# Kernel tuning notes

Hardware: AMD Instinct MI355X
Metric: run time of the kernel (lower is better)

The kernel has to match this reference:

```python
import jax, jax.numpy as jnp
import numpy as np

B, N, H, T = 4096, 512, 1024, 10  # batch, input_size, hidden_size, num_iterations
NUM_OPS = 20


def setup_inputs() -> dict:
    key = jax.random.key(0)
    k1, k2, k3, k4 = jax.random.split(key, 4)
    return {
        "x": jax.random.normal(k1, (B, N, 1), jnp.float32),
        "frozen_weight": jax.random.normal(k2, (1, N, H), jnp.float32) / np.sqrt(H),
        "alpha": jax.random.normal(k3, (T, NUM_OPS), jnp.float32),
        "layer_beta": jax.random.normal(k4, (T, 2), jnp.float32),
    }


def _softshrink(x, lam):
    return jnp.where(x > lam, x - lam, jnp.where(x < -lam, x + lam, jnp.zeros_like(x)))


def _hardshrink(x, lam):
    return jnp.where(jnp.abs(x) > lam, x, jnp.zeros_like(x))


def _make_ops(lam):
    # Same 20 ops, same order as the torch ModuleList.
    return [
        lambda x: _softshrink(x, lam),                 # Softshrink(0.001/L)
        jax.nn.relu,                                   # ReLU
        lambda x: x,                                   # Identity
        lambda x: jax.nn.gelu(x, approximate=False),   # GELU (exact erf, torch default)
        jax.nn.elu,                                    # ELU
        lambda x: _hardshrink(x, lam),                 # Hardshrink(0.001/L)
        lambda x: jnp.clip(x, -1.0, 1.0),              # Hardtanh
        jax.nn.hard_swish,                             # Hardswish
        jax.nn.selu,                                   # SELU
        jax.nn.celu,                                   # CELU
        jax.nn.leaky_relu,                             # LeakyReLU (slope 0.01)
        jax.nn.log_sigmoid,                            # LogSigmoid
        lambda x: x - jnp.tanh(x),                     # Tanhshrink
        jax.nn.soft_sign,                              # Softsign
        jax.nn.softplus,                               # Softplus
        jnp.tanh,                                      # Tanh
        jax.nn.sigmoid,                                # Sigmoid
        jax.nn.hard_sigmoid,                           # Hardsigmoid
        jax.nn.silu,                                   # SiLU
        lambda x: x * jnp.tanh(jax.nn.softplus(x)),    # Mish
    ]


def _forward(x, frozen_weight, alpha, layer_beta):
    W = frozen_weight[0]                       # [N, H]
    L = jnp.linalg.norm(W, ord=2) ** 2         # spectral norm squared (Lipschitz)
    lam = 0.001 / L
    ops = _make_ops(lam)

    b = x.shape[0]
    hidden = W.shape[1]
    z = jnp.zeros((b, hidden, 1), dtype=x.dtype)
    z_prev = z
    num_iters = alpha.shape[0]
    for i in range(num_iters):
        aw = jax.nn.softmax(alpha[i])          # [20] (training path, eval_flag=False)
        bw = jax.nn.softmax(layer_beta[i])     # [2]
        # FISTA-style momentum + frozen-weight gradient step
        z_aux = z + (i / (i + 3)) * (z - z_prev)      # [B,H,1]
        Wz = jnp.einsum('nh,bho->bno', W, z_aux)      # [B,N,1]
        grad = jnp.einsum('nh,bno->bho', W, Wz - x)   # [B,H,1]
        z_g = z_aux - grad / L
        # 20-way weighted activation mixture
        z_op = aw[0] * ops[0](z_g)
        for w, op in zip(aw[1:], ops[1:]):
            z_op = z_op + w * op(z_g)
        # beta-weighted residual mix becomes z_prev; z_op becomes current_z
        z_prev = z * bw[0] + z_op * bw[1]
        z = z_op
    return z


def reference(x, frozen_weight, alpha, layer_beta):
    return _forward(x, frozen_weight, alpha, layer_beta)
```

## Files before the change

kernel.cpp:

```cpp
#include <hip/hip_runtime.h>
#include <hip/hip_bf16.h>

#define DI __device__ __forceinline__

typedef float f32x4 __attribute__((ext_vector_type(4)));
typedef __bf16 bf16x8 __attribute__((ext_vector_type(8)));
using bf16_t = __hip_bfloat16;
using ushort_t = unsigned short;

DI void gload_lds16(const void* g, void* l) {
  __builtin_amdgcn_global_load_lds(
      (const __attribute__((address_space(1))) void*)g,
      (__attribute__((address_space(3))) void*)l, 16, 0, 0);
}

DI float rcpf(float x) { return __builtin_amdgcn_rcpf(x); }

DI float act_mix(float x, const float* aw, float lam) {
  const float ax  = fabsf(x);
  const float en  = __expf(-ax);
  const float en2 = en * en;
  const float i1  = rcpf(1.0f + en);
  const float sig = (x >= 0.0f) ? i1 : en * i1;
  const float th  = copysignf((1.0f - en2) * rcpf(1.0f + en2), x);
  const float l1p = __logf(1.0f + en);
  const float sp  = fmaxf(x, 0.0f) + l1p;
  const float lsg = fminf(x, 0.0f) - l1p;
  const float q   = ((x >= 0.0f) ? en2 : 1.0f) * (i1 * i1);
  const float mish = x * (1.0f - q) * rcpf(1.0f + q);
  const float u  = 0.7071067811865476f * x;
  const float au = fabsf(u);
  const float t  = rcpf(1.0f + 0.3275911f * au);
  float poly = fmaf(t, 1.061405429f, -1.453152027f);
  poly = fmaf(t, poly, 1.421413741f);
  poly = fmaf(t, poly, -0.284496736f);
  poly = fmaf(t, poly, 0.254829592f);
  poly *= t;
  const float erfa = 1.0f - poly * __expf(-u * u);
  const float gelu = 0.5f * x * (1.0f + copysignf(erfa, x));
  const float em1  = en - 1.0f;
  const float elu  = (x > 0.0f) ? x : em1;
  const float selu = (x > 0.0f) ? 1.0507009873554805f * x : 1.7580993408473766f * em1;
  const float relu = fmaxf(x, 0.0f);
  const float t6   = fminf(fmaxf(x + 3.0f, 0.0f), 6.0f) * 0.16666666666666666f;
  const float ssh  = (x > lam) ? (x - lam) : ((x < -lam) ? (x + lam) : 0.0f);
  const float hsh  = (ax > lam) ? x : 0.0f;
  const float htan = fminf(fmaxf(x, -1.0f), 1.0f);
  const float lky  = (x >= 0.0f) ? x : 0.01f * x;
  const float ssn  = x * rcpf(1.0f + ax);
  float r = aw[0] * ssh;
  r = fmaf(aw[1],  relu,   r);
  r = fmaf(aw[2],  x,      r);
  r = fmaf(aw[3],  gelu,   r);
  r = fmaf(aw[4],  elu,    r);
  r = fmaf(aw[5],  hsh,    r);
  r = fmaf(aw[6],  htan,   r);
  r = fmaf(aw[7],  x * t6, r);
  r = fmaf(aw[8],  selu,   r);
  r = fmaf(aw[9],  elu,    r);
  r = fmaf(aw[10], lky,    r);
  r = fmaf(aw[11], lsg,    r);
  r = fmaf(aw[12], x - th, r);
  r = fmaf(aw[13], ssn,    r);
  r = fmaf(aw[14], sp,     r);
  r = fmaf(aw[15], th,     r);
  r = fmaf(aw[16], sig,    r);
  r = fmaf(aw[17], t6,     r);
  r = fmaf(aw[18], x * sig, r);
  r = fmaf(aw[19], mish,   r);
  return r;
}

__global__ void k_prep(const float* __restrict__ W, const float* __restrict__ x,
                       bf16_t* __restrict__ Whi, bf16_t* __restrict__ Wlo,
                       bf16_t* __restrict__ Wth, bf16_t* __restrict__ Wtl,
                       bf16_t* __restrict__ xh, bf16_t* __restrict__ xl) {
  int i = blockIdx.x * 256 + threadIdx.x;
  if (i < 512 * 1024) {
    float w = W[i];
    bf16_t h = __float2bfloat16(w);
    bf16_t l = __float2bfloat16(w - __bfloat162float(h));
    Whi[i] = h; Wlo[i] = l;
    int n = i >> 10, hc = i & 1023;
    Wth[hc * 512 + n] = h; Wtl[hc * 512 + n] = l;
  }
  int j = i - 512 * 1024;
  if (j >= 0 && j < 4096 * 512) {
    float v = x[j];
    bf16_t h = __float2bfloat16(v);
    xh[j] = h;
    xl[j] = __float2bfloat16(v - __bfloat162float(h));
  }
}

template <int KDIM, bool FIRST, bool WF32>
__global__ __launch_bounds__(256) void k_sqm(
    const bf16_t* __restrict__ Xhi, const bf16_t* __restrict__ Xlo,
    bf16_t* __restrict__ Chi, bf16_t* __restrict__ Clo,
    float* __restrict__ Cf,
    const float* __restrict__ pin, float* __restrict__ pout) {
  __shared__ __align__(16) ushort_t Ah[2][32 * 64], Al[2][32 * 64],
                                    Bh[2][32 * 64], Bl[2][32 * 64];
  __shared__ float red[4];
  const int tid = threadIdx.x, lane = tid & 63, wave = tid >> 6;
  const int wm = wave >> 1, wn = wave & 1;
  const int i0 = blockIdx.x * 32, j0 = blockIdx.y * 32;
  const int bid = blockIdx.y * gridDim.x + blockIdx.x;
  const int r16 = lane & 15, kg = lane >> 4;

  float s = 1.0f;
  if constexpr (!FIRST) {
    float v = pin[tid];
    for (int off = 32; off; off >>= 1) v += __shfl_down(v, off, 64);
    if ((tid & 63) == 0) red[tid >> 6] = v;
    __syncthreads();
    s = 1.0f / (red[0] + red[1] + red[2] + red[3]);
    __syncthreads();
  }

  const int row = tid >> 3;
  const int srcc = (((tid & 7) ^ (row & 7)) << 3);
  const long abase = (long)(i0 + row) * KDIM + srcc;
  const long bbase = (long)(j0 + row) * KDIM + srcc;
  const int ldst = tid * 8;

  auto stage = [&](int buf, int kt) {
    gload_lds16(Xhi + abase + kt, &Ah[buf][ldst]);
    gload_lds16(Xlo + abase + kt, &Al[buf][ldst]);
    gload_lds16(Xhi + bbase + kt, &Bh[buf][ldst]);
    gload_lds16(Xlo + bbase + kt, &Bl[buf][ldst]);
  };

  f32x4 acc = {};
  constexpr int NT = KDIM / 64;
  stage(0, 0);
  __syncthreads();
  for (int t = 0; t < NT; ++t) {
    if (t + 1 < NT) stage((t + 1) & 1, (t + 1) * 64);
    const int b = t & 1;
    const int ra = wm * 16 + r16, rb = wn * 16 + r16;
#pragma unroll
    for (int kk = 0; kk < 64; kk += 32) {
      int oa = ra * 64 + ((kk + kg * 8) ^ ((ra & 7) * 8));
      int ob = rb * 64 + ((kk + kg * 8) ^ ((rb & 7) * 8));
      bf16x8 ah = *(const bf16x8*)&Ah[b][oa];
      bf16x8 al = *(const bf16x8*)&Al[b][oa];
      bf16x8 bh = *(const bf16x8*)&Bh[b][ob];
      bf16x8 bl = *(const bf16x8*)&Bl[b][ob];
      acc = __builtin_amdgcn_mfma_f32_16x16x32_bf16(ah, bh, acc, 0, 0, 0);
      acc = __builtin_amdgcn_mfma_f32_16x16x32_bf16(ah, bl, acc, 0, 0, 0);
      acc = __builtin_amdgcn_mfma_f32_16x16x32_bf16(al, bh, acc, 0, 0, 0);
    }
    __syncthreads();
  }

  float fro = 0.0f;
#pragma unroll
  for (int r = 0; r < 4; ++r) {
    float c = acc[r] * s;
    int orow = i0 + wm * 16 + (lane >> 4) * 4 + r;
    int ocol = j0 + wn * 16 + r16;
    int idx = orow * 512 + ocol;
    bf16_t h = __float2bfloat16(c);
    Chi[idx] = h;
    Clo[idx] = __float2bfloat16(c - __bfloat162float(h));
    if constexpr (WF32) Cf[idx] = c;
    fro = fmaf(c, c, fro);
  }
  for (int off = 32; off; off >>= 1) fro += __shfl_down(fro, off, 64);
  if ((tid & 63) == 0) red[tid >> 6] = fro;
  __syncthreads();
  if (tid == 0) pout[bid] = red[0] + red[1] + red[2] + red[3];
}

__global__ __launch_bounds__(256) void k_G(const bf16_t* __restrict__ Xhi,
                                           const bf16_t* __restrict__ Xlo,
                                           bf16_t* __restrict__ G) {
  __shared__ __align__(16) ushort_t Ah[2][32 * 64], Al[2][32 * 64],
                                    Bh[2][32 * 64], Bl[2][32 * 64];
  const int tid = threadIdx.x, lane = tid & 63, wave = tid >> 6;
  const int wm = wave >> 1, wn = wave & 1;
  const int i0 = blockIdx.x * 32, j0 = blockIdx.y * 32;
  const int r16 = lane & 15, kg = lane >> 4;
  const int row = tid >> 3;
  const int srcc = (((tid & 7) ^ (row & 7)) << 3);
  const long abase = (long)(i0 + row) * 512 + srcc;
  const long bbase = (long)(j0 + row) * 512 + srcc;
  const int ldst = tid * 8;

  auto stage = [&](int buf, int kt) {
    gload_lds16(Xhi + abase + kt, &Ah[buf][ldst]);
    gload_lds16(Xlo + abase + kt, &Al[buf][ldst]);
    gload_lds16(Xhi + bbase + kt, &Bh[buf][ldst]);
    gload_lds16(Xlo + bbase + kt, &Bl[buf][ldst]);
  };

  f32x4 acc = {};
  stage(0, 0);
  __syncthreads();
  for (int t = 0; t < 8; ++t) {
    if (t + 1 < 8) stage((t + 1) & 1, (t + 1) * 64);
    const int b = t & 1;
    const int ra = wm * 16 + r16, rb = wn * 16 + r16;
#pragma unroll
    for (int kk = 0; kk < 64; kk += 32) {
      int oa = ra * 64 + ((kk + kg * 8) ^ ((ra & 7) * 8));
      int ob = rb * 64 + ((kk + kg * 8) ^ ((rb & 7) * 8));
      bf16x8 ah = *(const bf16x8*)&Ah[b][oa];
      bf16x8 al = *(const bf16x8*)&Al[b][oa];
      bf16x8 bh = *(const bf16x8*)&Bh[b][ob];
      bf16x8 bl = *(const bf16x8*)&Bl[b][ob];
      acc = __builtin_amdgcn_mfma_f32_16x16x32_bf16(ah, bh, acc, 0, 0, 0);
      acc = __builtin_amdgcn_mfma_f32_16x16x32_bf16(ah, bl, acc, 0, 0, 0);
      acc = __builtin_amdgcn_mfma_f32_16x16x32_bf16(al, bh, acc, 0, 0, 0);
    }
    __syncthreads();
  }
#pragma unroll
  for (int r = 0; r < 4; ++r) {
    int orow = i0 + wm * 16 + (lane >> 4) * 4 + r;
    int ocol = j0 + wn * 16 + r16;
    G[orow * 1024 + ocol] = __float2bfloat16(acc[r]);
  }
}

__global__ __launch_bounds__(256) void k_xw(const bf16_t* __restrict__ xh_,
                                            const bf16_t* __restrict__ xl_,
                                            const bf16_t* __restrict__ Bh_,
                                            const bf16_t* __restrict__ Bl_,
                                            const float* __restrict__ prm,
                                            bf16_t* __restrict__ out,
                                            bf16_t* __restrict__ zB,
                                            bf16_t* __restrict__ zaux1) {
  __shared__ __align__(16) ushort_t Axh[2][64 * 64], Axl[2][64 * 64],
                                    Bwh[2][64 * 64], Bwl[2][64 * 64];
  const int tid = threadIdx.x, lane = tid & 63, wave = tid >> 6;
  const int wm = wave >> 1, wn = wave & 1;
  const int m0 = blockIdx.x * 64, n0 = blockIdx.y * 64;
  const int r16 = lane & 15, kg = lane >> 4;

  auto stage = [&](int buf, int kt) {
#pragma unroll
    for (int q = 0; q < 2; ++q) {
      int lin = (tid + q * 256) * 8;
      int row = lin >> 6;
      int col = ((((lin >> 3) & 7) ^ (row & 7)) << 3);
      gload_lds16(xh_ + (long)(m0 + row) * 512 + kt + col, &Axh[buf][lin]);
      gload_lds16(xl_ + (long)(m0 + row) * 512 + kt + col, &Axl[buf][lin]);
      gload_lds16(Bh_ + (long)(n0 + row) * 512 + kt + col, &Bwh[buf][lin]);
      gload_lds16(Bl_ + (long)(n0 + row) * 512 + kt + col, &Bwl[buf][lin]);
    }
  };

  f32x4 acc[2][2] = {};
  stage(0, 0);
  __syncthreads();
  for (int t = 0; t < 8; ++t) {
    if (t + 1 < 8) stage((t + 1) & 1, (t + 1) * 64);
    const int b = t & 1;
#pragma unroll
    for (int kk = 0; kk < 64; kk += 32) {
      bf16x8 ah[2], al[2], bh[2], bl[2];
#pragma unroll
      for (int f = 0; f < 2; ++f) {
        int ra = wm * 32 + f * 16 + r16;
        int rb = wn * 32 + f * 16 + r16;
        int oa = ra * 64 + ((kk + kg * 8) ^ ((ra & 7) * 8));
        int ob = rb * 64 + ((kk + kg * 8) ^ ((rb & 7) * 8));
        ah[f] = *(const bf16x8*)&Axh[b][oa];
        al[f] = *(const bf16x8*)&Axl[b][oa];
        bh[f] = *(const bf16x8*)&Bwh[b][ob];
        bl[f] = *(const bf16x8*)&Bwl[b][ob];
      }
#pragma unroll
      for (int i = 0; i < 2; ++i)
#pragma unroll
        for (int j = 0; j < 2; ++j) {
          acc[i][j] = __builtin_amdgcn_mfma_f32_16x16x32_bf16(ah[i], bh[j], acc[i][j], 0, 0, 0);
          acc[i][j] = __builtin_amdgcn_mfma_f32_16x16x32_bf16(ah[i], bl[j], acc[i][j], 0, 0, 0);
          acc[i][j] = __builtin_amdgcn_mfma_f32_16x16x32_bf16(al[i], bh[j], acc[i][j], 0, 0, 0);
        }
    }
    __syncthreads();
  }
  const float invL = prm[21];
  const float d0 = prm[20];
  const float lam = prm[22];
  float aw[20];
#pragma unroll
  for (int k = 0; k < 20; ++k) aw[k] = prm[k];
#pragma unroll
  for (int i = 0; i < 2; ++i)
#pragma unroll
    for (int j = 0; j < 2; ++j)
#pragma unroll
      for (int r = 0; r < 4; ++r) {
        int row = m0 + wm * 32 + i * 16 + (lane >> 4) * 4 + r;
        int col = n0 + wn * 32 + j * 16 + r16;
        long idx = (long)row * 1024 + col;
        bf16_t xb = __float2bfloat16(acc[i][j][r] * invL);
        out[idx] = xb;
        float zop = act_mix(__bfloat162float(xb), aw, lam);
        zB[idx] = __float2bfloat16(zop);
        zaux1[idx] = __float2bfloat16(zop * (1.0f + d0));
      }
}

__global__ __launch_bounds__(256) void k_dot(const float* __restrict__ A0,
                                             const float* __restrict__ B,
                                             float* __restrict__ numP,
                                             float* __restrict__ denP) {
  __shared__ float redn[4], redd[4];
  const int tid = threadIdx.x;
  const int idx4 = blockIdx.x * 256 + tid;
  const f32x4 a = ((const f32x4*)A0)[idx4];
  const f32x4 b = ((const f32x4*)B)[idx4];
  float nv = a[0]*b[0] + a[1]*b[1] + a[2]*b[2] + a[3]*b[3];
  float dv = 0.0f;
#pragma unroll
  for (int q = 0; q < 4; ++q) {
    int i = idx4 * 4 + q;
    if ((i >> 9) == (i & 511)) dv += b[q];
  }
  for (int off = 32; off; off >>= 1) {
    nv += __shfl_down(nv, off, 64);
    dv += __shfl_down(dv, off, 64);
  }
  if ((tid & 63) == 0) { redn[tid >> 6] = nv; redd[tid >> 6] = dv; }
  __syncthreads();
  if (tid == 0) {
    numP[blockIdx.x] = redn[0] + redn[1] + redn[2] + redn[3];
    denP[blockIdx.x] = redd[0] + redd[1] + redd[2] + redd[3];
  }
}

__global__ __launch_bounds__(256) void k_setup(const float* __restrict__ alpha,
                                               const float* __restrict__ beta,
                                               const float* __restrict__ numP,
                                               const float* __restrict__ denP,
                                               float* __restrict__ params) {
  __shared__ float redn[4], redd[4];
  __shared__ float Lsh;
  const int tid = threadIdx.x;
  float nv = numP[tid], dv = denP[tid];
  for (int off = 32; off; off >>= 1) {
    nv += __shfl_down(nv, off, 64);
    dv += __shfl_down(dv, off, 64);
  }
  if ((tid & 63) == 0) { redn[tid >> 6] = nv; redd[tid >> 6] = dv; }
  __syncthreads();
  if (tid == 0)
    Lsh = (redn[0] + redn[1] + redn[2] + redn[3]) /
          (redd[0] + redd[1] + redd[2] + redd[3]);
  __syncthreads();
  const int t = tid;
  if (t >= 10) return;
  float L = Lsh;
  float invL = 1.0f / L;
  float lam = 0.001f * invL;
  const float* a = alpha + t * 20;
  float mx = a[0];
  for (int k = 1; k < 20; ++k) mx = fmaxf(mx, a[k]);
  float e[20], ssum = 0.0f;
  for (int k = 0; k < 20; ++k) { e[k] = expf(a[k] - mx); ssum += e[k]; }
  float inv = 1.0f / ssum;
  float* P = params + t * 32;
  for (int k = 0; k < 20; ++k) P[k] = e[k] * inv;
  float b0 = beta[t * 2], b1 = beta[t * 2 + 1];
  float bm = fmaxf(b0, b1);
  float eb0 = expf(b0 - bm), eb1 = expf(b1 - bm);
  float bw0 = eb0 / (eb0 + eb1);
  P[20] = ((float)(t + 1) / (float)(t + 4)) * bw0;
  P[21] = invL;
  P[22] = lam;
  P[23] = L;
}

template <bool LAST>
__global__ __launch_bounds__(256, 3) void k_iter(const bf16_t* __restrict__ A,
                                                 const bf16_t* __restrict__ G,
                                                 const bf16_t* __restrict__ xWs,
                                                 bf16_t* __restrict__ zauxN,
                                                 bf16_t* zB, float* zio,
                                                 const float* __restrict__ prm) {
  __shared__ __align__(16) ushort_t As[3][64 * 64], Bs[3][64 * 64];
  const int tid = threadIdx.x, lane = tid & 63, wave = tid >> 6;
  const int wm = wave >> 1, wn = wave & 1;
  const int bid = blockIdx.x;
  const int swz = (bid & 7) * 128 + (bid >> 3);
  const int m0 = (swz >> 4) * 64, n0 = (swz & 15) * 64;
  const int r16 = lane & 15, kg = lane >> 4;

  auto stage = [&](int buf, int kt) {
#pragma unroll
    for (int q = 0; q < 2; ++q) {
      int lin = (tid + q * 256) * 8;
      int row = lin >> 6;
      int col = ((((lin >> 3) & 7) ^ (row & 7)) << 3);
      gload_lds16(A + (long)(m0 + row) * 1024 + kt + col, &As[buf][lin]);
      gload_lds16(G + (long)(n0 + row) * 1024 + kt + col, &Bs[buf][lin]);
    }
  };

  f32x4 acc[2][2] = {};
  auto compute = [&](int b) {
#pragma unroll
    for (int kk = 0; kk < 64; kk += 32) {
      bf16x8 a[2], bb[2];
#pragma unroll
      for (int f = 0; f < 2; ++f) {
        int ra = wm * 32 + f * 16 + r16;
        int rb = wn * 32 + f * 16 + r16;
        a[f]  = *(const bf16x8*)&As[b][ra * 64 + ((kk + kg * 8) ^ ((ra & 7) * 8))];
        bb[f] = *(const bf16x8*)&Bs[b][rb * 64 + ((kk + kg * 8) ^ ((rb & 7) * 8))];
      }
#pragma unroll
      for (int i = 0; i < 2; ++i)
#pragma unroll
        for (int j = 0; j < 2; ++j)
          acc[i][j] = __builtin_amdgcn_mfma_f32_16x16x32_bf16(a[i], bb[j], acc[i][j], 0, 0, 0);
    }
  };

  stage(0, 0);
  stage(1, 64);
  stage(2, 128);
  asm volatile("s_waitcnt vmcnt(8)" ::: "memory");
  __builtin_amdgcn_s_barrier();
  __builtin_amdgcn_sched_barrier(0);

  for (int t = 0; t < 16; ++t) {
    compute(t % 3);
    if (t == 15) break;
    asm volatile("s_waitcnt lgkmcnt(0)" ::: "memory");
    __builtin_amdgcn_sched_barrier(0);
    __builtin_amdgcn_s_barrier();
    if (t + 3 < 16) {
      stage(t % 3, (t + 3) * 64);
      asm volatile("s_waitcnt vmcnt(8)" ::: "memory");
    } else if (t == 13) {
      asm volatile("s_waitcnt vmcnt(4)" ::: "memory");
    } else {
      asm volatile("s_waitcnt vmcnt(0)" ::: "memory");
    }
    __builtin_amdgcn_s_barrier();
    __builtin_amdgcn_sched_barrier(0);
  }
  __builtin_amdgcn_sched_barrier(0);

  const float d_i = prm[20];
  const float invL = prm[21];
  const float lam = prm[22];
  float aw[20];
#pragma unroll
  for (int k = 0; k < 20; ++k) aw[k] = prm[k];

  float xv[2][2][4], av[2][2][4], zv[2][2][4];
#pragma unroll
  for (int i = 0; i < 2; ++i)
#pragma unroll
    for (int j = 0; j < 2; ++j)
#pragma unroll
      for (int r = 0; r < 4; ++r) {
        int row = m0 + wm * 32 + i * 16 + (lane >> 4) * 4 + r;
        int col = n0 + wn * 32 + j * 16 + r16;
        long idx = (long)row * 1024 + col;
        xv[i][j][r] = __bfloat162float(xWs[idx]);
        av[i][j][r] = __bfloat162float(A[idx]);
        if (!LAST) zv[i][j][r] = __bfloat162float(zB[idx]);
      }
#pragma unroll
  for (int i = 0; i < 2; ++i)
#pragma unroll
    for (int j = 0; j < 2; ++j)
#pragma unroll
      for (int r = 0; r < 4; ++r) {
        int row = m0 + wm * 32 + i * 16 + (lane >> 4) * 4 + r;
        int col = n0 + wn * 32 + j * 16 + r16;
        long idx = (long)row * 1024 + col;
        float zg = fmaf(-acc[i][j][r], invL, av[i][j][r] + xv[i][j][r]);
        float zop = act_mix(zg, aw, lam);
        if (LAST) {
          zio[idx] = zop;
        } else {
          zB[idx] = __float2bfloat16(zop);
          zauxN[idx] = __float2bfloat16(fmaf(d_i, zop - zv[i][j][r], zop));
        }
      }
}

extern "C" void kernel_launch(void* const* d_in, const int* in_sizes, int n_in,
                              void* d_out, int out_size, void* d_ws, size_t ws_size,
                              hipStream_t stream) {
  const float* x     = (const float*)d_in[0];
  const float* W     = (const float*)d_in[1];
  const float* alpha = (const float*)d_in[2];
  const float* beta  = (const float*)d_in[3];
  float* zout = (float*)d_out;

  char* ws = (char*)d_ws;
  const size_t MB = 1u << 20;
  float* pb[11];
  for (int k = 0; k < 11; ++k) pb[k] = (float*)(ws + (size_t)k * 1024);
  float* numP   = (float*)(ws + 12 * 1024);
  float* denP   = (float*)(ws + 13 * 1024);
  float* params = (float*)(ws + 14 * 1024);
  const size_t HDR = 32768;
  float*  A0f  = (float*)(ws + HDR);
  float*  Bf   = (float*)(ws + HDR + 1 * MB);
  bf16_t* H0   = (bf16_t*)(ws + HDR + 2 * MB);
  bf16_t* L0   = (bf16_t*)(ws + HDR + 2 * MB + 512 * 1024);
  bf16_t* H1   = (bf16_t*)(ws + HDR + 3 * MB);
  bf16_t* L1   = (bf16_t*)(ws + HDR + 3 * MB + 512 * 1024);
  bf16_t* Whi  = (bf16_t*)(ws + HDR + 4 * MB);
  bf16_t* Wlo  = (bf16_t*)(ws + HDR + 5 * MB);
  bf16_t* Wth  = (bf16_t*)(ws + HDR + 6 * MB);
  bf16_t* Wtl  = (bf16_t*)(ws + HDR + 7 * MB);
  bf16_t* Gm   = (bf16_t*)(ws + HDR + 8 * MB);
  bf16_t* xh   = (bf16_t*)(ws + HDR + 10 * MB);
  bf16_t* xl   = (bf16_t*)(ws + HDR + 14 * MB);
  bf16_t* xWs  = (bf16_t*)(ws + HDR + 18 * MB);
  bf16_t* zx0  = (bf16_t*)(ws + HDR + 26 * MB);
  bf16_t* zx1  = (bf16_t*)(ws + HDR + 34 * MB);
  bf16_t* zB   = (bf16_t*)(ws + HDR + 42 * MB);

  k_prep<<<10240, 256, 0, stream>>>(W, x, Whi, Wlo, Wth, Wtl, xh, xl);

  k_sqm<1024, true, true><<<dim3(16, 16), 256, 0, stream>>>(
      Whi, Wlo, H0, L0, A0f, nullptr, pb[0]);
  bf16_t* Hs[2] = {H0, H1};
  bf16_t* Ls[2] = {L0, L1};
  int pp = 0;
  for (int k = 0; k < 9; ++k) {
    if (k == 8)
      k_sqm<512, false, true><<<dim3(16, 16), 256, 0, stream>>>(
          Hs[pp], Ls[pp], Hs[pp ^ 1], Ls[pp ^ 1], Bf, pb[k], pb[k + 1]);
    else
      k_sqm<512, false, false><<<dim3(16, 16), 256, 0, stream>>>(
          Hs[pp], Ls[pp], Hs[pp ^ 1], Ls[pp ^ 1], nullptr, pb[k], pb[k + 1]);
    pp ^= 1;
  }
  k_dot<<<256, 256, 0, stream>>>(A0f, Bf, numP, denP);
  k_setup<<<1, 256, 0, stream>>>(alpha, beta, numP, denP, params);

  k_G<<<dim3(32, 32), 256, 0, stream>>>(Wth, Wtl, Gm);
  k_xw<<<dim3(64, 16), 256, 0, stream>>>(xh, xl, Wth, Wtl, params, xWs, zB, zx1);

  bf16_t* zx[2] = {zx0, zx1};
  for (int i = 1; i < 9; ++i)
    k_iter<false><<<1024, 256, 0, stream>>>(zx[i & 1], Gm, xWs, zx[(i + 1) & 1],
                                            zB, zout, params + i * 32);
  k_iter<true><<<1024, 256, 0, stream>>>(zx[9 & 1], Gm, xWs, zx0 ,
                                         zB, zout, params + 9 * 32);
}
```

Before: 405.5 us.

## Use single-bf16 xW GEMM with k_iter pipeline and double-buffer iteration GEMM

Converts x to a single bf16 array instead of a hi/lo split and computes x·W with one MFMA per tile instead of three. The xW kernel now shares the k_iter-style pipelined, swizzled 1D-grid structure. k_iter drops from triple to double buffering, with launch bounds raised to 4 blocks per CU for occupancy. This cuts MFMA work and memory traffic for the x·W product, at the cost of lower precision there and less prefetch depth in the iteration GEMM.

```diff
diff --git a/kernel.cpp b/kernel.cpp
--- a/kernel.cpp
+++ b/kernel.cpp
@@ -74,7 +74,7 @@
 __global__ void k_prep(const float* __restrict__ W, const float* __restrict__ x,
                        bf16_t* __restrict__ Whi, bf16_t* __restrict__ Wlo,
                        bf16_t* __restrict__ Wth, bf16_t* __restrict__ Wtl,
-                       bf16_t* __restrict__ xh, bf16_t* __restrict__ xl) {
+                       bf16_t* __restrict__ xb) {
   int i = blockIdx.x * 256 + threadIdx.x;
   if (i < 512 * 1024) {
     float w = W[i];
@@ -85,12 +85,7 @@
     Wth[hc * 512 + n] = h; Wtl[hc * 512 + n] = l;
   }
   int j = i - 512 * 1024;
-  if (j >= 0 && j < 4096 * 512) {
-    float v = x[j];
-    bf16_t h = __float2bfloat16(v);
-    xh[j] = h;
-    xl[j] = __float2bfloat16(v - __bfloat162float(h));
-  }
+  if (j >= 0 && j < 4096 * 512) xb[j] = __float2bfloat16(x[j]);
 }
 
 template <int KDIM, bool FIRST, bool WF32>
@@ -222,88 +217,6 @@
     int ocol = j0 + wn * 16 + r16;
     G[orow * 1024 + ocol] = __float2bfloat16(acc[r]);
   }
-}
-
-__global__ __launch_bounds__(256) void k_xw(const bf16_t* __restrict__ xh_,
-                                            const bf16_t* __restrict__ xl_,
-                                            const bf16_t* __restrict__ Bh_,
-                                            const bf16_t* __restrict__ Bl_,
-                                            const float* __restrict__ prm,
-                                            bf16_t* __restrict__ out,
-                                            bf16_t* __restrict__ zB,
-                                            bf16_t* __restrict__ zaux1) {
-  __shared__ __align__(16) ushort_t Axh[2][64 * 64], Axl[2][64 * 64],
-                                    Bwh[2][64 * 64], Bwl[2][64 * 64];
-  const int tid = threadIdx.x, lane = tid & 63, wave = tid >> 6;
-  const int wm = wave >> 1, wn = wave & 1;
-  const int m0 = blockIdx.x * 64, n0 = blockIdx.y * 64;
-  const int r16 = lane & 15, kg = lane >> 4;
-
-  auto stage = [&](int buf, int kt) {
-#pragma unroll
-    for (int q = 0; q < 2; ++q) {
-      int lin = (tid + q * 256) * 8;
-      int row = lin >> 6;
-      int col = ((((lin >> 3) & 7) ^ (row & 7)) << 3);
-      gload_lds16(xh_ + (long)(m0 + row) * 512 + kt + col, &Axh[buf][lin]);
-      gload_lds16(xl_ + (long)(m0 + row) * 512 + kt + col, &Axl[buf][lin]);
-      gload_lds16(Bh_ + (long)(n0 + row) * 512 + kt + col, &Bwh[buf][lin]);
-      gload_lds16(Bl_ + (long)(n0 + row) * 512 + kt + col, &Bwl[buf][lin]);
-    }
-  };
-
-  f32x4 acc[2][2] = {};
-  stage(0, 0);
-  __syncthreads();
-  for (int t = 0; t < 8; ++t) {
-    if (t + 1 < 8) stage((t + 1) & 1, (t + 1) * 64);
-    const int b = t & 1;
-#pragma unroll
-    for (int kk = 0; kk < 64; kk += 32) {
-      bf16x8 ah[2], al[2], bh[2], bl[2];
-#pragma unroll
-      for (int f = 0; f < 2; ++f) {
-        int ra = wm * 32 + f * 16 + r16;
-        int rb = wn * 32 + f * 16 + r16;
-        int oa = ra * 64 + ((kk + kg * 8) ^ ((ra & 7) * 8));
-        int ob = rb * 64 + ((kk + kg * 8) ^ ((rb & 7) * 8));
-        ah[f] = *(const bf16x8*)&Axh[b][oa];
-        al[f] = *(const bf16x8*)&Axl[b][oa];
-        bh[f] = *(const bf16x8*)&Bwh[b][ob];
-        bl[f] = *(const bf16x8*)&Bwl[b][ob];
-      }
-#pragma unroll
-      for (int i = 0; i < 2; ++i)
-#pragma unroll
-        for (int j = 0; j < 2; ++j) {
-          acc[i][j] = __builtin_amdgcn_mfma_f32_16x16x32_bf16(ah[i], bh[j], acc[i][j], 0, 0, 0);
-          acc[i][j] = __builtin_amdgcn_mfma_f32_16x16x32_bf16(ah[i], bl[j], acc[i][j], 0, 0, 0);
-          acc[i][j] = __builtin_amdgcn_mfma_f32_16x16x32_bf16(al[i], bh[j], acc[i][j], 0, 0, 0);
-        }
-    }
-    __syncthreads();
-  }
-  const float invL = prm[21];
-  const float d0 = prm[20];
-  const float lam = prm[22];
-  float aw[20];
-#pragma unroll
-  for (int k = 0; k < 20; ++k) aw[k] = prm[k];
-#pragma unroll
-  for (int i = 0; i < 2; ++i)
-#pragma unroll
-    for (int j = 0; j < 2; ++j)
-#pragma unroll
-      for (int r = 0; r < 4; ++r) {
-        int row = m0 + wm * 32 + i * 16 + (lane >> 4) * 4 + r;
-        int col = n0 + wn * 32 + j * 16 + r16;
-        long idx = (long)row * 1024 + col;
-        bf16_t xb = __float2bfloat16(acc[i][j][r] * invL);
-        out[idx] = xb;
-        float zop = act_mix(__bfloat162float(xb), aw, lam);
-        zB[idx] = __float2bfloat16(zop);
-        zaux1[idx] = __float2bfloat16(zop * (1.0f + d0));
-      }
 }
 
 __global__ __launch_bounds__(256) void k_dot(const float* __restrict__ A0,
@@ -376,14 +289,13 @@
   P[23] = L;
 }
 
-template <bool LAST>
-__global__ __launch_bounds__(256, 3) void k_iter(const bf16_t* __restrict__ A,
-                                                 const bf16_t* __restrict__ G,
-                                                 const bf16_t* __restrict__ xWs,
-                                                 bf16_t* __restrict__ zauxN,
-                                                 bf16_t* zB, float* zio,
-                                                 const float* __restrict__ prm) {
-  __shared__ __align__(16) ushort_t As[3][64 * 64], Bs[3][64 * 64];
+__global__ __launch_bounds__(256, 4) void k_xw(const bf16_t* __restrict__ xb,
+                                               const bf16_t* __restrict__ Wth,
+                                               const float* __restrict__ prm,
+                                               bf16_t* __restrict__ out,
+                                               bf16_t* __restrict__ zB,
+                                               bf16_t* __restrict__ zaux1) {
+  __shared__ __align__(16) ushort_t As[2][64 * 64], Bs[2][64 * 64];
   const int tid = threadIdx.x, lane = tid & 63, wave = tid >> 6;
   const int wm = wave >> 1, wn = wave & 1;
   const int bid = blockIdx.x;
@@ -397,8 +309,8 @@
       int lin = (tid + q * 256) * 8;
       int row = lin >> 6;
       int col = ((((lin >> 3) & 7) ^ (row & 7)) << 3);
-      gload_lds16(A + (long)(m0 + row) * 1024 + kt + col, &As[buf][lin]);
-      gload_lds16(G + (long)(n0 + row) * 1024 + kt + col, &Bs[buf][lin]);
+      gload_lds16(xb + (long)(m0 + row) * 512 + kt + col, &As[buf][lin]);
+      gload_lds16(Wth + (long)(n0 + row) * 512 + kt + col, &Bs[buf][lin]);
     }
   };
 
@@ -424,21 +336,110 @@
 
   stage(0, 0);
   stage(1, 64);
-  stage(2, 128);
-  asm volatile("s_waitcnt vmcnt(8)" ::: "memory");
+  asm volatile("s_waitcnt vmcnt(4)" ::: "memory");
   __builtin_amdgcn_s_barrier();
   __builtin_amdgcn_sched_barrier(0);
 
+  for (int t = 0; t < 8; ++t) {
+    compute(t & 1);
+    if (t == 7) break;
+    asm volatile("s_waitcnt lgkmcnt(0)" ::: "memory");
+    __builtin_amdgcn_sched_barrier(0);
+    __builtin_amdgcn_s_barrier();
+    if (t + 2 < 8) {
+      stage(t & 1, (t + 2) * 64);
+      asm volatile("s_waitcnt vmcnt(4)" ::: "memory");
+    } else {
+      asm volatile("s_waitcnt vmcnt(0)" ::: "memory");
+    }
+    __builtin_amdgcn_s_barrier();
+    __builtin_amdgcn_sched_barrier(0);
+  }
+  __builtin_amdgcn_sched_barrier(0);
+
+  const float invL = prm[21];
+  const float d0 = prm[20];
+  const float lam = prm[22];
+  float aw[20];
+#pragma unroll
+  for (int k = 0; k < 20; ++k) aw[k] = prm[k];
+#pragma unroll
+  for (int i = 0; i < 2; ++i)
+#pragma unroll
+    for (int j = 0; j < 2; ++j)
+#pragma unroll
+      for (int r = 0; r < 4; ++r) {
+        int row = m0 + wm * 32 + i * 16 + (lane >> 4) * 4 + r;
+        int col = n0 + wn * 32 + j * 16 + r16;
+        long idx = (long)row * 1024 + col;
+        bf16_t xv = __float2bfloat16(acc[i][j][r] * invL);
+        out[idx] = xv;
+        float zop = act_mix(__bfloat162float(xv), aw, lam);
+        zB[idx] = __float2bfloat16(zop);
+        zaux1[idx] = __float2bfloat16(zop * (1.0f + d0));
+      }
+}
+
+template <bool LAST>
+__global__ __launch_bounds__(256, 4) void k_iter(const bf16_t* __restrict__ A,
+                                                 const bf16_t* __restrict__ G,
+                                                 const bf16_t* __restrict__ xWs,
+                                                 bf16_t* __restrict__ zauxN,
+                                                 bf16_t* zB, float* zio,
+                                                 const float* __restrict__ prm) {
+  __shared__ __align__(16) ushort_t As[2][64 * 64], Bs[2][64 * 64];
+  const int tid = threadIdx.x, lane = tid & 63, wave = tid >> 6;
+  const int wm = wave >> 1, wn = wave & 1;
+  const int bid = blockIdx.x;
+  const int swz = (bid & 7) * 128 + (bid >> 3);
+  const int m0 = (swz >> 4) * 64, n0 = (swz & 15) * 64;
+  const int r16 = lane & 15, kg = lane >> 4;
+
+  auto stage = [&](int buf, int kt) {
+#pragma unroll
+    for (int q = 0; q < 2; ++q) {
+      int lin = (tid + q * 256) * 8;
+      int row = lin >> 6;
+      int col = ((((lin >> 3) & 7) ^ (row & 7)) << 3);
+      gload_lds16(A + (long)(m0 + row) * 1024 + kt + col, &As[buf][lin]);
+      gload_lds16(G + (long)(n0 + row) * 1024 + kt + col, &Bs[buf][lin]);
+    }
+  };
+
+  f32x4 acc[2][2] = {};
+  auto compute = [&](int b) {
+#pragma unroll
+    for (int kk = 0; kk < 64; kk += 32) {
+      bf16x8 a[2], bb[2];
+#pragma unroll
+      for (int f = 0; f < 2; ++f) {
+        int ra = wm * 32 + f * 16 + r16;
+        int rb = wn * 32 + f * 16 + r16;
+        a[f]  = *(const bf16x8*)&As[b][ra * 64 + ((kk + kg * 8) ^ ((ra & 7) * 8))];
+        bb[f] = *(const bf16x8*)&Bs[b][rb * 64 + ((kk + kg * 8) ^ ((rb & 7) * 8))];
+      }
+#pragma unroll
+      for (int i = 0; i < 2; ++i)
+#pragma unroll
+        for (int j = 0; j < 2; ++j)
+          acc[i][j] = __builtin_amdgcn_mfma_f32_16x16x32_bf16(a[i], bb[j], acc[i][j], 0, 0, 0);
+    }
+  };
+
+  stage(0, 0);
+  stage(1, 64);
+  asm volatile("s_waitcnt vmcnt(4)" ::: "memory");
+  __builtin_amdgcn_s_barrier();
+  __builtin_amdgcn_sched_barrier(0);
+
   for (int t = 0; t < 16; ++t) {
-    compute(t % 3);
+    compute(t & 1);
     if (t == 15) break;
     asm volatile("s_waitcnt lgkmcnt(0)" ::: "memory");
     __builtin_amdgcn_sched_barrier(0);
     __builtin_amdgcn_s_barrier();
-    if (t + 3 < 16) {
-      stage(t % 3, (t + 3) * 64);
-      asm volatile("s_waitcnt vmcnt(8)" ::: "memory");
-    } else if (t == 13) {
+    if (t + 2 < 16) {
+      stage(t & 1, (t + 2) * 64);
       asm volatile("s_waitcnt vmcnt(4)" ::: "memory");
     } else {
       asm volatile("s_waitcnt vmcnt(0)" ::: "memory");
@@ -517,14 +518,13 @@
   bf16_t* Wth  = (bf16_t*)(ws + HDR + 6 * MB);
   bf16_t* Wtl  = (bf16_t*)(ws + HDR + 7 * MB);
   bf16_t* Gm   = (bf16_t*)(ws + HDR + 8 * MB);
-  bf16_t* xh   = (bf16_t*)(ws + HDR + 10 * MB);
-  bf16_t* xl   = (bf16_t*)(ws + HDR + 14 * MB);
+  bf16_t* xb   = (bf16_t*)(ws + HDR + 10 * MB);
   bf16_t* xWs  = (bf16_t*)(ws + HDR + 18 * MB);
   bf16_t* zx0  = (bf16_t*)(ws + HDR + 26 * MB);
   bf16_t* zx1  = (bf16_t*)(ws + HDR + 34 * MB);
   bf16_t* zB   = (bf16_t*)(ws + HDR + 42 * MB);
 
-  k_prep<<<10240, 256, 0, stream>>>(W, x, Whi, Wlo, Wth, Wtl, xh, xl);
+  k_prep<<<10240, 256, 0, stream>>>(W, x, Whi, Wlo, Wth, Wtl, xb);
 
   k_sqm<1024, true, true><<<dim3(16, 16), 256, 0, stream>>>(
       Whi, Wlo, H0, L0, A0f, nullptr, pb[0]);
@@ -544,7 +544,7 @@
   k_setup<<<1, 256, 0, stream>>>(alpha, beta, numP, denP, params);
 
   k_G<<<dim3(32, 32), 256, 0, stream>>>(Wth, Wtl, Gm);
-  k_xw<<<dim3(64, 16), 256, 0, stream>>>(xh, xl, Wth, Wtl, params, xWs, zB, zx1);
+  k_xw<<<1024, 256, 0, stream>>>(xb, Wth, params, xWs, zB, zx1);
 
   bf16_t* zx[2] = {zx0, zx1};
   for (int i = 1; i < 9; ++i)
```

After: 369.1 us. 1.1x faster.
